# Optimization experiments

Measured on AMD Instinct MI355X. Metric: run time of the kernel, lower is better.

The kernel has to match this reference:

```python
import jax, jax.numpy as jnp
import numpy as np

NUM_NODES = 100000
NUM_EDGES = 1600000
IN_DIM = 128
OUT_DIM = 128


def setup_inputs() -> dict:
    key = jax.random.key(0)
    k_x, k_e, k_wn, k_bn, k_ws, k_bs = jax.random.split(key, 6)
    x = jax.random.normal(k_x, (NUM_NODES, IN_DIM), dtype=jnp.float32)
    edge_index = jax.random.randint(k_e, (2, NUM_EDGES), 0, NUM_NODES, dtype=jnp.int64)
    s = 1.0 / np.sqrt(IN_DIM)
    W_neigh = jax.random.uniform(k_wn, (OUT_DIM, IN_DIM), dtype=jnp.float32, minval=-s, maxval=s)
    b_neigh = jax.random.uniform(k_bn, (OUT_DIM,), dtype=jnp.float32, minval=-s, maxval=s)
    W_self = jax.random.uniform(k_ws, (OUT_DIM, IN_DIM), dtype=jnp.float32, minval=-s, maxval=s)
    b_self = jax.random.uniform(k_bs, (OUT_DIM,), dtype=jnp.float32, minval=-s, maxval=s)
    return {"x": x, "edge_index": edge_index, "W_neigh": W_neigh, "b_neigh": b_neigh,
            "W_self": W_self, "b_self": b_self}


def reference(x, edge_index, W_neigh, b_neigh, W_self, b_self):
    src, dst = edge_index[0], edge_index[1]
    # gather source node feats per edge, sum-aggregate per destination node
    msgs = x[src]  # [E, d]
    neigh = jax.ops.segment_sum(msgs, dst, num_segments=x.shape[0])  # [N, d]
    neigh_proj = neigh @ W_neigh.T + b_neigh  # [N, out]
    self_proj = x @ W_self.T + b_self         # [N, out]
    return neigh_proj + self_proj
```

## Files before the change

kernel.cpp:

```cpp
#include <hip/hip_runtime.h>
#include <hip/hip_bf16.h>

#define NN 100000
#define NE 1600000
#define DIM 128
#define BM 64
#define CAP 28
#define OVFCAP 2048
#define CVT_BLK 1024
#define SC_BLK 2048
#define SLICE 12544
#define FGRID 1568

typedef __attribute__((ext_vector_type(8))) short short8;
typedef __attribute__((ext_vector_type(4))) float f32x4;
typedef __attribute__((ext_vector_type(4))) unsigned short ushort4v;
typedef __attribute__((ext_vector_type(4))) int int4v;

__device__ __forceinline__ unsigned short f2bf(float f) {
  union { float f; unsigned u; } v; v.f = f;
  unsigned r = v.u + 0x7fffu + ((v.u >> 16) & 1u);
  return (unsigned short)(r >> 16);
}
__device__ __forceinline__ float bf2f(unsigned short h) {
  union { unsigned u; float f; } v; v.u = ((unsigned)h) << 16;
  return v.f;
}

__global__ __launch_bounds__(256) void prep_scatter_kernel(
    const float* __restrict__ x, const int* __restrict__ ei,
    const float* __restrict__ Wn, const float* __restrict__ bn,
    const float* __restrict__ Ws, const float* __restrict__ bs,
    unsigned short* __restrict__ xb, unsigned short* __restrict__ wnb,
    unsigned short* __restrict__ wsb, float* __restrict__ bsum,
    int* __restrict__ cnt, int* __restrict__ ovfcnt, int2* __restrict__ ovf,
    int* __restrict__ slots) {
  int b = blockIdx.x;
  if (b < CVT_BLK) {
    const int slice = b & 7;
    const int tid_g = (b >> 3) * 256 + threadIdx.x;
    const int r0 = slice * SLICE;
    const int r1 = min(r0 + SLICE, NN);
    const int i0 = r0 * (DIM / 4), i1 = r1 * (DIM / 4);
    for (int i = i0 + tid_g; i < i1; i += 128 * 256) {
      f32x4 v = reinterpret_cast<const f32x4*>(x)[i];
      ushort4v u;
      u[0] = f2bf(v[0]); u[1] = f2bf(v[1]); u[2] = f2bf(v[2]); u[3] = f2bf(v[3]);
      reinterpret_cast<ushort4v*>(xb)[i] = u;
    }
    if (slice == 0) {
      if (tid_g < DIM * DIM) { wnb[tid_g] = f2bf(Wn[tid_g]); wsb[tid_g] = f2bf(Ws[tid_g]); }
      if (tid_g < DIM) bsum[tid_g] = bn[tid_g] + bs[tid_g];
    }
  } else {
    const int sb  = b - CVT_BLK;
    const int sl  = sb & 7;
    const int lo  = sl * SLICE;
    const int hi  = min(lo + SLICE, NN);
    const int rng = hi - lo;
    const int tid_g = (sb >> 3) * 256 + threadIdx.x;
    const int STR = 256 * 256;
    const int NCH = NE / 4;
    for (int c = tid_g; c < NCH; c += STR) {
      int4v d4 = *reinterpret_cast<const int4v*>(ei + NE + 4 * c);
      #pragma unroll
      for (int j = 0; j < 4; ++j) {
        int d = d4[j];
        if ((unsigned)(d - lo) < (unsigned)rng) {
          int s = ei[4 * c + j];
          if ((unsigned)s >= NN) continue;
          int r = atomicAdd(&cnt[d], 1);
          if (r < CAP) {
            slots[d * CAP + r] = s;
          } else {
            int o = atomicAdd(&ovfcnt[sl], 1);
            if (o < OVFCAP) ovf[sl * OVFCAP + o] = make_int2(d, s);
          }
        }
      }
    }
  }
}

__global__ __launch_bounds__(512) void fusedgemm_kernel(
    const unsigned short* __restrict__ xb,
    const int* __restrict__ cnt, const int* __restrict__ slots,
    const int2* __restrict__ ovf, const int* __restrict__ ovfcnt,
    const unsigned short* __restrict__ wnb, const unsigned short* __restrict__ wsb,
    const float* __restrict__ bsum, float* __restrict__ out) {
  __shared__ unsigned short sW[64 * DIM];
  __shared__ unsigned short sA[BM * DIM];
  __shared__ unsigned short sX[BM * DIM];
  __shared__ int2 lovf[256];
  __shared__ int lovfn;
  const int tid = threadIdx.x;
  const int slice = blockIdx.x & 7;
  const int row0 = slice * SLICE + (blockIdx.x >> 3) * BM;
  if (row0 >= NN) return;

  if (tid == 0) lovfn = 0;
  #pragma unroll
  for (int it = 0; it < 2; ++it) {
    int id = it * 512 + tid;
    int r = id >> 4, c = id & 15;
    int gr = row0 + r;
    short8 v = (short8)0;
    if (gr < NN) v = *reinterpret_cast<const short8*>(xb + (size_t)gr * DIM + c * 8);
    int off = (r * 256 + c * 16) ^ ((r & 7) << 4);
    *reinterpret_cast<short8*>(reinterpret_cast<char*>(sX) + off) = v;
  }
  {
    int id = tid;
    #pragma unroll
    for (int it = 0; it < 2; ++it, id += 512) {
      int r = id >> 4, c = id & 15;
      short8 w = *reinterpret_cast<const short8*>(wnb + r * DIM + c * 8);
      int off = (r * 256 + c * 16) ^ ((r & 7) << 4);
      *reinterpret_cast<short8*>(reinterpret_cast<char*>(sW) + off) = w;
    }
  }
  __syncthreads();

  {
    int ovfn = min(ovfcnt[slice], OVFCAP);
    const int2* osl = ovf + slice * OVFCAP;
    for (int k = tid; k < ovfn; k += 512) {
      int2 p = osl[k];
      if ((unsigned)(p.x - row0) < (unsigned)BM) {
        int t = atomicAdd(&lovfn, 1);
        if (t < 256) lovf[t] = p;
      }
    }
  }
  __syncthreads();

  {
    const int lg = tid >> 5, ln = tid & 31;
    int g = row0 + lg;
    int m = 0, idx = 0;
    if (g < NN) {
      m = min(cnt[g], CAP);
      if (ln < m) idx = slots[g * CAP + ln];
    }
    const int lcnt = min(lovfn, 256);
    for (int it = 0; it < 4; ++it) {
      int r = it * 16 + lg;
      int gcur = row0 + r;
      int mn = 0, idxn = 0;
      if (it < 3) {
        int gn = row0 + (it + 1) * 16 + lg;
        if (gn < NN) {
          mn = min(cnt[gn], CAP);
          if (ln < mn) idxn = slots[gn * CAP + ln];
        }
      }
      f32x4 a0 = (f32x4){0.f,0.f,0.f,0.f}, a1 = a0, a2 = a0, a3 = a0;
      f32x4 a4 = a0, a5 = a0, a6 = a0, a7 = a0;
      int e = 0;
      for (; e + 7 < m; e += 8) {
        int s0 = __shfl(idx, e, 32),     s1 = __shfl(idx, e + 1, 32);
        int s2 = __shfl(idx, e + 2, 32), s3 = __shfl(idx, e + 3, 32);
        int s4 = __shfl(idx, e + 4, 32), s5 = __shfl(idx, e + 5, 32);
        int s6 = __shfl(idx, e + 6, 32), s7 = __shfl(idx, e + 7, 32);
        ushort4v u0 = *reinterpret_cast<const ushort4v*>(xb + (size_t)s0 * DIM + ln * 4);
        ushort4v u1 = *reinterpret_cast<const ushort4v*>(xb + (size_t)s1 * DIM + ln * 4);
        ushort4v u2 = *reinterpret_cast<const ushort4v*>(xb + (size_t)s2 * DIM + ln * 4);
        ushort4v u3 = *reinterpret_cast<const ushort4v*>(xb + (size_t)s3 * DIM + ln * 4);
        ushort4v u4 = *reinterpret_cast<const ushort4v*>(xb + (size_t)s4 * DIM + ln * 4);
        ushort4v u5 = *reinterpret_cast<const ushort4v*>(xb + (size_t)s5 * DIM + ln * 4);
        ushort4v u6 = *reinterpret_cast<const ushort4v*>(xb + (size_t)s6 * DIM + ln * 4);
        ushort4v u7 = *reinterpret_cast<const ushort4v*>(xb + (size_t)s7 * DIM + ln * 4);
        #pragma unroll
        for (int j = 0; j < 4; ++j) {
          a0[j] += bf2f(u0[j]); a1[j] += bf2f(u1[j]);
          a2[j] += bf2f(u2[j]); a3[j] += bf2f(u3[j]);
          a4[j] += bf2f(u4[j]); a5[j] += bf2f(u5[j]);
          a6[j] += bf2f(u6[j]); a7[j] += bf2f(u7[j]);
        }
      }
      for (; e + 3 < m; e += 4) {
        int s0 = __shfl(idx, e, 32),     s1 = __shfl(idx, e + 1, 32);
        int s2 = __shfl(idx, e + 2, 32), s3 = __shfl(idx, e + 3, 32);
        ushort4v u0 = *reinterpret_cast<const ushort4v*>(xb + (size_t)s0 * DIM + ln * 4);
        ushort4v u1 = *reinterpret_cast<const ushort4v*>(xb + (size_t)s1 * DIM + ln * 4);
        ushort4v u2 = *reinterpret_cast<const ushort4v*>(xb + (size_t)s2 * DIM + ln * 4);
        ushort4v u3 = *reinterpret_cast<const ushort4v*>(xb + (size_t)s3 * DIM + ln * 4);
        #pragma unroll
        for (int j = 0; j < 4; ++j) {
          a0[j] += bf2f(u0[j]); a1[j] += bf2f(u1[j]);
          a2[j] += bf2f(u2[j]); a3[j] += bf2f(u3[j]);
        }
      }
      for (; e < m; ++e) {
        int s0 = __shfl(idx, e, 32);
        ushort4v u0 = *reinterpret_cast<const ushort4v*>(xb + (size_t)s0 * DIM + ln * 4);
        #pragma unroll
        for (int j = 0; j < 4; ++j) a0[j] += bf2f(u0[j]);
      }
      for (int k2 = 0; k2 < lcnt; ++k2) {
        int2 p = lovf[k2];
        if (p.x == gcur) {
          ushort4v u0 = *reinterpret_cast<const ushort4v*>(xb + (size_t)p.y * DIM + ln * 4);
          #pragma unroll
          for (int j = 0; j < 4; ++j) a0[j] += bf2f(u0[j]);
        }
      }
      a0 += a1; a2 += a3; a4 += a5; a6 += a7;
      a0 += a2; a4 += a6; a0 += a4;
      ushort4v o;
      o[0] = f2bf(a0[0]); o[1] = f2bf(a0[1]); o[2] = f2bf(a0[2]); o[3] = f2bf(a0[3]);
      int off = (r * 256 + ln * 8) ^ ((r & 7) << 4);
      *reinterpret_cast<ushort4v*>(reinterpret_cast<char*>(sA) + off) = o;
      idx = idxn; m = mn;
    }
  }
  __syncthreads();

  const int wave = tid >> 6;
  const int lane = tid & 63;
  const int wm = wave & 3, wn = wave >> 2;
  const int arow = wm * 16 + (lane & 15);
  const int kl = (lane >> 4) * 8;
  f32x4 acc[4];
  #pragma unroll
  for (int t = 0; t < 4; ++t) acc[t] = (f32x4){0.f, 0.f, 0.f, 0.f};

  #pragma unroll
  for (int st = 0; st < 4; ++st) {
    const bool self = st >= 2;
    const int  tbase = (st & 1) * 2;
    #pragma unroll
    for (int ks = 0; ks < 4; ++ks) {
      int k = ks * 32 + kl;
      short8 a;
      if (!self)
        a = *reinterpret_cast<const short8*>(
            reinterpret_cast<const char*>(sA) + ((arow * 256 + k * 2) ^ ((arow & 7) << 4)));
      else
        a = *reinterpret_cast<const short8*>(
            reinterpret_cast<const char*>(sX) + ((arow * 256 + k * 2) ^ ((arow & 7) << 4)));
      #pragma unroll
      for (int t = 0; t < 2; ++t) {
        int o = wn * 32 + t * 16 + (lane & 15);
        short8 bfr = *reinterpret_cast<const short8*>(
            reinterpret_cast<const char*>(sW) + ((o * 256 + k * 2) ^ ((o & 7) << 4)));
        acc[tbase + t] = __builtin_amdgcn_mfma_f32_16x16x32_bf16(a, bfr, acc[tbase + t], 0, 0, 0);
      }
    }
    if (st < 3) {
      __syncthreads();
      const unsigned short* wsrc = (st == 0) ? (wnb + 64 * DIM)
                                 : (st == 1) ? wsb : (wsb + 64 * DIM);
      int id = tid;
      #pragma unroll
      for (int it = 0; it < 2; ++it, id += 512) {
        int r = id >> 4, c = id & 15;
        short8 w = *reinterpret_cast<const short8*>(wsrc + r * DIM + c * 8);
        int off = (r * 256 + c * 16) ^ ((r & 7) << 4);
        *reinterpret_cast<short8*>(reinterpret_cast<char*>(sW) + off) = w;
      }
      __syncthreads();
    }
  }

  #pragma unroll
  for (int t = 0; t < 4; ++t) {
    int col = ((t >> 1) ? 64 : 0) + wn * 32 + (t & 1) * 16 + (lane & 15);
    float bv = bsum[col];
    #pragma unroll
    for (int reg = 0; reg < 4; ++reg) {
      int gr = row0 + wm * 16 + (lane >> 4) * 4 + reg;
      if (gr < NN) out[(size_t)gr * DIM + col] = acc[t][reg] + bv;
    }
  }
}

extern "C" void kernel_launch(void* const* d_in, const int* in_sizes, int n_in,
                              void* d_out, int out_size, void* d_ws, size_t ws_size,
                              hipStream_t stream) {
  const float* x  = (const float*)d_in[0];
  const int*   ei = (const int*)d_in[1];
  const float* Wn = (const float*)d_in[2];
  const float* bn = (const float*)d_in[3];
  const float* Ws = (const float*)d_in[4];
  const float* bs = (const float*)d_in[5];
  float* out = (float*)d_out;
  char* ws = (char*)d_ws;

  unsigned short* wnb = (unsigned short*)(ws + 0);
  unsigned short* wsb = (unsigned short*)(ws + 32768);
  float* bsum        = (float*)(ws + 65536);
  int* cnt           = (int*)(ws + 66560);
  int* ovfcnt        = (int*)(ws + 466560);
  int2* ovf          = (int2*)(ws + 466688);
  int* slots         = (int*)(ws + 597760);
  unsigned short* xb = (unsigned short*)(ws + 11797760);

  hipMemsetAsync(cnt, 0, 400064, stream);
  prep_scatter_kernel<<<CVT_BLK + SC_BLK, 256, 0, stream>>>(
      x, ei, Wn, bn, Ws, bs, xb, wnb, wsb, bsum, cnt, ovfcnt, ovf, slots);
  fusedgemm_kernel<<<FGRID, 512, 0, stream>>>(
      xb, cnt, slots, ovf, ovfcnt, wnb, wsb, bsum, out);
}
```

Baseline: 171.2 us.

## Bin edges by destination slice before scattering into CSR slots

Replaces the single scatter pass, where each of 8 slice groups re-read the whole destination array, with a two-phase scheme. First, edges are binned into 8 per-slice buckets through shared-memory staging and packed (dst offset, src) words. A separate scatter kernel then reads only its own slice's bucket. This cuts redundant edge-index reads and keeps the per-slice L2 locality of the count atomics, at the cost of an extra kernel launch and a bucket write/read pass that reuses the output buffer as scratch.

```diff
diff --git a/kernel.cpp b/kernel.cpp
--- a/kernel.cpp
+++ b/kernel.cpp
@@ -8,9 +8,12 @@
 #define CAP 28
 #define OVFCAP 2048
 #define CVT_BLK 1024
+#define BIN_BLK 1024
 #define SC_BLK 2048
 #define SLICE 12544
 #define FGRID 1568
+#define BUCKCAP 262144
+#define TILE 1024
 
 typedef __attribute__((ext_vector_type(8))) short short8;
 typedef __attribute__((ext_vector_type(4))) float f32x4;
@@ -27,14 +30,13 @@
   return v.f;
 }
 
-__global__ __launch_bounds__(256) void prep_scatter_kernel(
+__global__ __launch_bounds__(256) void cvt_bin_kernel(
     const float* __restrict__ x, const int* __restrict__ ei,
     const float* __restrict__ Wn, const float* __restrict__ bn,
     const float* __restrict__ Ws, const float* __restrict__ bs,
     unsigned short* __restrict__ xb, unsigned short* __restrict__ wnb,
     unsigned short* __restrict__ wsb, float* __restrict__ bsum,
-    int* __restrict__ cnt, int* __restrict__ ovfcnt, int2* __restrict__ ovf,
-    int* __restrict__ slots) {
+    int* __restrict__ gcur, unsigned* __restrict__ gbuf) {
   int b = blockIdx.x;
   if (b < CVT_BLK) {
     const int slice = b & 7;
@@ -53,29 +55,93 @@
       if (tid_g < DIM) bsum[tid_g] = bn[tid_g] + bs[tid_g];
     }
   } else {
-    const int sb  = b - CVT_BLK;
-    const int sl  = sb & 7;
-    const int lo  = sl * SLICE;
-    const int hi  = min(lo + SLICE, NN);
-    const int rng = hi - lo;
-    const int tid_g = (sb >> 3) * 256 + threadIdx.x;
-    const int STR = 256 * 256;
-    const int NCH = NE / 4;
-    for (int c = tid_g; c < NCH; c += STR) {
-      int4v d4 = *reinterpret_cast<const int4v*>(ei + NE + 4 * c);
+    const int bb = b - CVT_BLK;
+    const int tid = threadIdx.x;
+    __shared__ unsigned buf[8][TILE];
+    __shared__ int bcnt[8];
+    __shared__ int gbase[8];
+    const int NTILES = (NE + TILE - 1) / TILE;
+    for (int t = bb; t < NTILES; t += BIN_BLK) {
+      if (tid < 8) bcnt[tid] = 0;
+      __syncthreads();
+      int e0 = t * TILE + tid * 4;
+      if (e0 + 3 < NE) {
+        int4v s4 = *reinterpret_cast<const int4v*>(ei + e0);
+        int4v d4 = *reinterpret_cast<const int4v*>(ei + NE + e0);
+        #pragma unroll
+        for (int j = 0; j < 4; ++j) {
+          int s = s4[j], d = d4[j];
+          if ((unsigned)s < NN && (unsigned)d < NN) {
+            int sl = (unsigned)d / (unsigned)SLICE;
+            int pos = atomicAdd(&bcnt[sl], 1);
+            buf[sl][pos] = ((unsigned)(d - sl * SLICE) << 17) | (unsigned)s;
+          }
+        }
+      } else {
+        for (int j = 0; j < 4; ++j) {
+          int ee = e0 + j;
+          if (ee >= NE) break;
+          int s = ei[ee], d = ei[NE + ee];
+          if ((unsigned)s < NN && (unsigned)d < NN) {
+            int sl = (unsigned)d / (unsigned)SLICE;
+            int pos = atomicAdd(&bcnt[sl], 1);
+            buf[sl][pos] = ((unsigned)(d - sl * SLICE) << 17) | (unsigned)s;
+          }
+        }
+      }
+      __syncthreads();
+      if (tid < 8) gbase[tid] = atomicAdd(&gcur[tid], bcnt[tid]);
+      __syncthreads();
       #pragma unroll
-      for (int j = 0; j < 4; ++j) {
-        int d = d4[j];
-        if ((unsigned)(d - lo) < (unsigned)rng) {
-          int s = ei[4 * c + j];
-          if ((unsigned)s >= NN) continue;
-          int r = atomicAdd(&cnt[d], 1);
-          if (r < CAP) {
-            slots[d * CAP + r] = s;
-          } else {
-            int o = atomicAdd(&ovfcnt[sl], 1);
-            if (o < OVFCAP) ovf[sl * OVFCAP + o] = make_int2(d, s);
-          }
+      for (int s = 0; s < 8; ++s) {
+        int n = bcnt[s], gb = gbase[s];
+        for (int i = tid; i < n; i += 256) {
+          int gi = gb + i;
+          if (gi < BUCKCAP) gbuf[(size_t)s * BUCKCAP + gi] = buf[s][i];
+        }
+      }
+      __syncthreads();
+    }
+  }
+}
+
+__global__ __launch_bounds__(256) void scatter_kernel(
+    const unsigned* __restrict__ gbuf, const int* __restrict__ gcur,
+    int* __restrict__ cnt, int* __restrict__ ovfcnt, int2* __restrict__ ovf,
+    int* __restrict__ slots) {
+  const int sl = blockIdx.x & 7;
+  const int lo = sl * SLICE;
+  const int idx = blockIdx.x >> 3;
+  const int tid_g = idx * 256 + threadIdx.x;
+  const int n = min(gcur[sl], BUCKCAP);
+  const unsigned* bk = gbuf + (size_t)sl * BUCKCAP;
+  const int STR = 256 * 256;
+  for (int i0 = tid_g * 4; i0 < n; i0 += 4 * STR) {
+    unsigned e4[4];
+    int k = min(4, n - i0);
+    if (k == 4) {
+      int4v v = *reinterpret_cast<const int4v*>(bk + i0);
+      e4[0] = v[0]; e4[1] = v[1]; e4[2] = v[2]; e4[3] = v[3];
+    } else {
+      for (int j = 0; j < k; ++j) e4[j] = bk[i0 + j];
+    }
+    int rr[4], dd[4], ss[4];
+    #pragma unroll
+    for (int j = 0; j < 4; ++j) {
+      if (j < k) {
+        dd[j] = lo + (int)(e4[j] >> 17);
+        ss[j] = (int)(e4[j] & 0x1FFFFu);
+        rr[j] = atomicAdd(&cnt[dd[j]], 1);
+      }
+    }
+    #pragma unroll
+    for (int j = 0; j < 4; ++j) {
+      if (j < k) {
+        if (rr[j] < CAP) {
+          slots[dd[j] * CAP + rr[j]] = ss[j];
+        } else {
+          int o = atomicAdd(&ovfcnt[sl], 1);
+          if (o < OVFCAP) ovf[sl * OVFCAP + o] = make_int2(dd[j], ss[j]);
         }
       }
     }
@@ -145,7 +211,7 @@
     const int lcnt = min(lovfn, 256);
     for (int it = 0; it < 4; ++it) {
       int r = it * 16 + lg;
-      int gcur = row0 + r;
+      int gcur2 = row0 + r;
       int mn = 0, idxn = 0;
       if (it < 3) {
         int gn = row0 + (it + 1) * 16 + lg;
@@ -199,7 +265,7 @@
       }
       for (int k2 = 0; k2 < lcnt; ++k2) {
         int2 p = lovf[k2];
-        if (p.x == gcur) {
+        if (p.x == gcur2) {
           ushort4v u0 = *reinterpret_cast<const ushort4v*>(xb + (size_t)p.y * DIM + ln * 4);
           #pragma unroll
           for (int j = 0; j < 4; ++j) a0[j] += bf2f(u0[j]);
@@ -292,13 +358,18 @@
   float* bsum        = (float*)(ws + 65536);
   int* cnt           = (int*)(ws + 66560);
   int* ovfcnt        = (int*)(ws + 466560);
+  int* gcur          = (int*)(ws + 466592);
   int2* ovf          = (int2*)(ws + 466688);
   int* slots         = (int*)(ws + 597760);
   unsigned short* xb = (unsigned short*)(ws + 11797760);
 
+  unsigned* gbuf = (unsigned*)d_out;
+
   hipMemsetAsync(cnt, 0, 400064, stream);
-  prep_scatter_kernel<<<CVT_BLK + SC_BLK, 256, 0, stream>>>(
-      x, ei, Wn, bn, Ws, bs, xb, wnb, wsb, bsum, cnt, ovfcnt, ovf, slots);
+  cvt_bin_kernel<<<CVT_BLK + BIN_BLK, 256, 0, stream>>>(
+      x, ei, Wn, bn, Ws, bs, xb, wnb, wsb, bsum, gcur, gbuf);
+  scatter_kernel<<<SC_BLK, 256, 0, stream>>>(
+      gbuf, gcur, cnt, ovfcnt, ovf, slots);
   fusedgemm_kernel<<<FGRID, 512, 0, stream>>>(
       xb, cnt, slots, ovf, ovfcnt, wnb, wsb, bsum, out);
 }
```

Measured after the change: 197.8 us. 15.5% more time.
